# Performance work log

Measured on AMD Instinct MI355X. Metric: run time of the kernel, lower is better.

The kernel has to match this reference:

```python
import jax, jax.numpy as jnp
import numpy as np

SQ, B, NP, HN = 2048, 2, 16, 64  # [seq, batch, heads, head_dim]

def setup_inputs() -> dict:
    key = jax.random.key(0)
    kq, kk, kv = jax.random.split(key, 3)
    return {
        "query": jax.random.normal(kq, (SQ, B, NP, HN), dtype=jnp.float32),
        "key":   jax.random.normal(kk, (SQ, B, NP, HN), dtype=jnp.float32),
        "value": jax.random.normal(kv, (SQ, B, NP, HN), dtype=jnp.float32),
    }

def reference(query, key, value):
    sq, b, nheads, hn = query.shape
    # NOTE: original module computes norm_factor=sqrt(hn) but never applies it;
    # scores are UNscaled QK^T, replicated faithfully here.
    scores = jnp.einsum('sbnh,tbnh->bnst', query, key)          # [b, np, sq, sk]
    probs = jax.nn.softmax(scores, axis=-1)                      # mask=None -> plain softmax
    # dropout is deterministic (train=False default) -> identity
    context = jnp.einsum('bnst,tbnh->sbnh', probs, value)        # [sq, b, np, hn]
    return context.reshape(sq, b, nheads * hn).astype(jnp.float32)
```

## Files before the change

### kernel.cpp

```cpp
#include <hip/hip_runtime.h>
#include <math.h>
#include <stdint.h>

#define SQ 2048
#define NBH 32
#define HN 64
#define BQ 128
#define BK 64
#define NT (SQ/BK)
#define TOK 2048
#define HSTRIDE (SQ*HN)

typedef _Float16 half2v __attribute__((ext_vector_type(2)));
typedef _Float16 half4v __attribute__((ext_vector_type(4)));
typedef _Float16 half8v __attribute__((ext_vector_type(8)));
typedef float f32x16 __attribute__((ext_vector_type(16)));

__device__ __forceinline__ void async16(const void* g, void* l) {
  __builtin_amdgcn_global_load_lds(
      (const __attribute__((address_space(1))) void*)g,
      (__attribute__((address_space(3))) void*)l, 16, 0, 0);
}

__global__ __launch_bounds__(256) void prep_k(const float* __restrict__ K,
                                              _Float16* __restrict__ Kh) {
  const int t = threadIdx.x;
  const int head = blockIdx.y;
  const int key = blockIdx.x * 64 + (t >> 2);
  const int c0 = (t & 3) * 2;
  const float* src = K + (size_t)key * TOK + head * HN + c0 * 8;
  float4 a = *(const float4*)src;
  float4 b = *(const float4*)(src + 4);
  float4 c = *(const float4*)(src + 8);
  float4 d = *(const float4*)(src + 12);
  half8v h0, h1;
  h0[0]=(_Float16)a.x; h0[1]=(_Float16)a.y; h0[2]=(_Float16)a.z; h0[3]=(_Float16)a.w;
  h0[4]=(_Float16)b.x; h0[5]=(_Float16)b.y; h0[6]=(_Float16)b.z; h0[7]=(_Float16)b.w;
  h1[0]=(_Float16)c.x; h1[1]=(_Float16)c.y; h1[2]=(_Float16)c.z; h1[3]=(_Float16)c.w;
  h1[4]=(_Float16)d.x; h1[5]=(_Float16)d.y; h1[6]=(_Float16)d.z; h1[7]=(_Float16)d.w;
  _Float16* row = Kh + (size_t)head * HSTRIDE + (size_t)key * 64;
  *(half8v*)&row[((c0    ) ^ (key & 7)) * 8] = h0;
  *(half8v*)&row[((c0 + 1) ^ (key & 7)) * 8] = h1;
}

__global__ __launch_bounds__(256) void prep_v(const float* __restrict__ V,
                                              _Float16* __restrict__ Vt) {
  __shared__ _Float16 vs[HN * 64];
  const int t = threadIdx.x;
  const int head = blockIdx.y;
  const int kt = blockIdx.x * 64;
  const int kl = (t >> 3) * 2;
  const int db = (t & 7) * 8;
  const float* src = V + (size_t)(kt + kl) * TOK + head * HN + db;
  float4 a0 = *(const float4*)src;
  float4 a1 = *(const float4*)(src + 4);
  float4 b0 = *(const float4*)(src + TOK);
  float4 b1 = *(const float4*)(src + TOK + 4);
  const float av[8] = {a0.x,a0.y,a0.z,a0.w,a1.x,a1.y,a1.z,a1.w};
  const float bv[8] = {b0.x,b0.y,b0.z,b0.w,b1.x,b1.y,b1.z,b1.w};
  const int u = kl >> 2;
  #pragma unroll
  for (int j = 0; j < 8; ++j) {
    const int dim = db + j;
    const int pos = u ^ (dim & 15);
    half2v h; h[0] = (_Float16)av[j]; h[1] = (_Float16)bv[j];
    *(half2v*)&vs[dim * 64 + pos * 4 + (kl & 3)] = h;
  }
  __syncthreads();
  const int dim = t >> 2;
  const int q = (t & 3) ^ (dim & 3);
  const _Float16* srow = &vs[dim * 64 + q * 16];
  _Float16* drow = Vt + (size_t)head * HSTRIDE + (size_t)dim * SQ + kt + q * 16;
  *(half8v*)&drow[0] = *(const half8v*)&srow[0];
  *(half8v*)&drow[8] = *(const half8v*)&srow[8];
}

__global__ __launch_bounds__(256, 2)
void fattn_mfma(const float* __restrict__ Q, const _Float16* __restrict__ Kh,
                const _Float16* __restrict__ Vt, float* __restrict__ O) {
  __shared__ __align__(16) _Float16 kbf[2][BK * 64];
  __shared__ __align__(16) _Float16 vtf[2][HN * 64];

  const int t = threadIdx.x;
  const int lane = t & 63;
  const int w = t >> 6;
  const int h2 = lane >> 5;
  const int l31 = lane & 31;
  const int q0 = blockIdx.x * BQ + w * 32;
  const int head = blockIdx.y;
  const _Float16* Kp = Kh + (size_t)head * HSTRIDE;
  const _Float16* Vp = Vt + (size_t)head * HSTRIDE;

  half8v qf[4];
  {
    const float* qp = Q + (size_t)(q0 + l31) * TOK + head * HN + 8 * h2;
    #pragma unroll
    for (int ks = 0; ks < 4; ++ks) {
      float4 a = *(const float4*)(qp + 16 * ks);
      float4 b = *(const float4*)(qp + 16 * ks + 4);
      half8v f;
      f[0] = (_Float16)a.x; f[1] = (_Float16)a.y; f[2] = (_Float16)a.z; f[3] = (_Float16)a.w;
      f[4] = (_Float16)b.x; f[5] = (_Float16)b.y; f[6] = (_Float16)b.z; f[7] = (_Float16)b.w;
      qf[ks] = f;
    }
  }

  f32x16 acc0, acc1;
  #pragma unroll
  for (int r = 0; r < 16; ++r) { acc0[r] = 0.f; acc1[r] = 0.f; }
  float m_i = -INFINITY, l_i = 0.f;

  auto stage = [&](int it) {
    const int kt = it * BK;
    const int buf = it & 1;
    #pragma unroll
    for (int i = 0; i < 2; ++i) {
      const int off = w * 1024 + i * 512;
      async16(Kp + (size_t)kt * 64 + off + lane * 8, &kbf[buf][off]);
    }
    #pragma unroll
    for (int i = 0; i < 2; ++i) {
      const int off = w * 1024 + i * 512;
      const int eo = off + lane * 8;
      const int dim = eo >> 6, inner = eo & 63;
      async16(Vp + (size_t)dim * SQ + kt + inner, &vtf[buf][off]);
    }
  };

  stage(0);
  for (int it = 0; it < NT; ++it) {
    __syncthreads();
    if (it + 1 < NT) stage(it + 1);
    const int cur = it & 1;

    f32x16 sf0, sf1;
    {
      f32x16 c0, c1;
      #pragma unroll
      for (int r = 0; r < 16; ++r) { c0[r] = 0.f; c1[r] = 0.f; }
      #pragma unroll
      for (int ks = 0; ks < 4; ++ks) {
        const int pos = ((h2 + 2 * ks) ^ (l31 & 7)) * 8;
        half8v a0v = *(const half8v*)&kbf[cur][l31 * 64 + pos];
        half8v a1v = *(const half8v*)&kbf[cur][(l31 + 32) * 64 + pos];
        c0 = __builtin_amdgcn_mfma_f32_32x32x16_f16(a0v, qf[ks], c0, 0, 0, 0);
        c1 = __builtin_amdgcn_mfma_f32_32x32x16_f16(a1v, qf[ks], c1, 0, 0, 0);
      }
      sf0 = c0; sf1 = c1;
    }

    float mx = -INFINITY;
    #pragma unroll
    for (int r = 0; r < 16; ++r) mx = fmaxf(mx, fmaxf(sf0[r], sf1[r]));
    mx = fmaxf(mx, __shfl_xor(mx, 32, 64));
    const float mnew = fmaxf(m_i, mx);
    const float alpha = __expf(m_i - mnew);
    float rsum = 0.f;
    #pragma unroll
    for (int r = 0; r < 16; ++r) {
      float p0 = __expf(sf0[r] - mnew);
      float p1 = __expf(sf1[r] - mnew);
      sf0[r] = p0; sf1[r] = p1;
      rsum += p0 + p1;
    }
    rsum += __shfl_xor(rsum, 32, 64);
    l_i = l_i * alpha + rsum;
    m_i = mnew;
    #pragma unroll
    for (int r = 0; r < 16; ++r) { acc0[r] *= alpha; acc1[r] *= alpha; }

    #pragma unroll
    for (int ks = 0; ks < 4; ++ks) {
      const int rb = 8 * (ks & 1);
      const f32x16& s = (ks < 2) ? sf0 : sf1;
      union { half8v v8; half2v v2[4]; } pu;
      #pragma unroll
      for (int tt = 0; tt < 4; ++tt) {
        auto pk = __builtin_amdgcn_cvt_pkrtz(s[rb + 2 * tt], s[rb + 2 * tt + 1]);
        pu.v2[tt] = *(half2v*)&pk;
      }
      #pragma unroll
      for (int mbd = 0; mbd < 2; ++mbd) {
        const int dim = l31 + 32 * mbd;
        const int sw = dim & 15;
        union { half8v v8; half4v v4[2]; } au;
        au.v4[0] = *(const half4v*)&vtf[cur][dim * 64 + ((4 * ks + h2)     ^ sw) * 4];
        au.v4[1] = *(const half4v*)&vtf[cur][dim * 64 + ((4 * ks + 2 + h2) ^ sw) * 4];
        if (mbd == 0)
          acc0 = __builtin_amdgcn_mfma_f32_32x32x16_f16(au.v8, pu.v8, acc0, 0, 0, 0);
        else
          acc1 = __builtin_amdgcn_mfma_f32_32x32x16_f16(au.v8, pu.v8, acc1, 0, 0, 0);
      }
    }
  }

  const float invl = 1.f / l_i;
  float* orow = O + (size_t)(q0 + l31) * TOK + head * HN;
  #pragma unroll
  for (int r = 0; r < 16; ++r) {
    const int d = (r & 3) + 8 * (r >> 2) + 4 * h2;
    orow[d]      = acc0[r] * invl;
    orow[d + 32] = acc1[r] * invl;
  }
}

extern "C" void kernel_launch(void* const* d_in, const int* in_sizes, int n_in,
                              void* d_out, int out_size, void* d_ws, size_t ws_size,
                              hipStream_t stream) {
  const float* Q = (const float*)d_in[0];
  const float* K = (const float*)d_in[1];
  const float* V = (const float*)d_in[2];
  float* O = (float*)d_out;
  _Float16* Kh = (_Float16*)d_ws;
  _Float16* Vh = Kh + (size_t)NBH * HSTRIDE;
  prep_k<<<dim3(SQ / 64, NBH), 256, 0, stream>>>(K, Kh);
  prep_v<<<dim3(SQ / 64, NBH), 256, 0, stream>>>(V, Vh);
  fattn_mfma<<<dim3(SQ / BQ, NBH), 256, 0, stream>>>(Q, Kh, Vh, O);
}
```

Measured before the change: 159.7 us.

## Process 128 keys per iteration, use exp2 with prescaled Q, fuse K/V prep kernels

The attention loop now handles two 64-key tiles per iteration, which halves the number of barriers and online-softmax rescale steps and doubles the LDS staging buffers. Q is prescaled by log2(e) so the exponentials can use the native exp2 instruction. The separate K and V conversion kernels are merged into one launch to cut launch overhead. The cost is higher register and LDS use, which may lower occupancy, plus a small extra fp16 rounding from the prescaled Q.

```diff
diff --git a/kernel.cpp b/kernel.cpp
--- a/kernel.cpp
+++ b/kernel.cpp
@@ -7,7 +7,8 @@
 #define HN 64
 #define BQ 128
 #define BK 64
-#define NT (SQ/BK)
+#define BK2 128
+#define NP2 (SQ/BK2)
 #define TOK 2048
 #define HSTRIDE (SQ*HN)
 
@@ -22,64 +23,72 @@
       (__attribute__((address_space(3))) void*)l, 16, 0, 0);
 }
 
-__global__ __launch_bounds__(256) void prep_k(const float* __restrict__ K,
-                                              _Float16* __restrict__ Kh) {
-  const int t = threadIdx.x;
-  const int head = blockIdx.y;
-  const int key = blockIdx.x * 64 + (t >> 2);
-  const int c0 = (t & 3) * 2;
-  const float* src = K + (size_t)key * TOK + head * HN + c0 * 8;
-  float4 a = *(const float4*)src;
-  float4 b = *(const float4*)(src + 4);
-  float4 c = *(const float4*)(src + 8);
-  float4 d = *(const float4*)(src + 12);
-  half8v h0, h1;
-  h0[0]=(_Float16)a.x; h0[1]=(_Float16)a.y; h0[2]=(_Float16)a.z; h0[3]=(_Float16)a.w;
-  h0[4]=(_Float16)b.x; h0[5]=(_Float16)b.y; h0[6]=(_Float16)b.z; h0[7]=(_Float16)b.w;
-  h1[0]=(_Float16)c.x; h1[1]=(_Float16)c.y; h1[2]=(_Float16)c.z; h1[3]=(_Float16)c.w;
-  h1[4]=(_Float16)d.x; h1[5]=(_Float16)d.y; h1[6]=(_Float16)d.z; h1[7]=(_Float16)d.w;
-  _Float16* row = Kh + (size_t)head * HSTRIDE + (size_t)key * 64;
-  *(half8v*)&row[((c0    ) ^ (key & 7)) * 8] = h0;
-  *(half8v*)&row[((c0 + 1) ^ (key & 7)) * 8] = h1;
-}
-
-__global__ __launch_bounds__(256) void prep_v(const float* __restrict__ V,
-                                              _Float16* __restrict__ Vt) {
+__device__ __forceinline__ float fexp2(float x) {
+#if __has_builtin(__builtin_amdgcn_exp2f)
+  return __builtin_amdgcn_exp2f(x);
+#else
+  return exp2f(x);
+#endif
+}
+
+__global__ __launch_bounds__(256) void prep_kv(const float* __restrict__ K,
+                                               const float* __restrict__ V,
+                                               _Float16* __restrict__ Kh,
+                                               _Float16* __restrict__ Vt) {
   __shared__ _Float16 vs[HN * 64];
   const int t = threadIdx.x;
   const int head = blockIdx.y;
-  const int kt = blockIdx.x * 64;
-  const int kl = (t >> 3) * 2;
-  const int db = (t & 7) * 8;
-  const float* src = V + (size_t)(kt + kl) * TOK + head * HN + db;
-  float4 a0 = *(const float4*)src;
-  float4 a1 = *(const float4*)(src + 4);
-  float4 b0 = *(const float4*)(src + TOK);
-  float4 b1 = *(const float4*)(src + TOK + 4);
-  const float av[8] = {a0.x,a0.y,a0.z,a0.w,a1.x,a1.y,a1.z,a1.w};
-  const float bv[8] = {b0.x,b0.y,b0.z,b0.w,b1.x,b1.y,b1.z,b1.w};
-  const int u = kl >> 2;
-  #pragma unroll
-  for (int j = 0; j < 8; ++j) {
-    const int dim = db + j;
-    const int pos = u ^ (dim & 15);
-    half2v h; h[0] = (_Float16)av[j]; h[1] = (_Float16)bv[j];
-    *(half2v*)&vs[dim * 64 + pos * 4 + (kl & 3)] = h;
-  }
-  __syncthreads();
-  const int dim = t >> 2;
-  const int q = (t & 3) ^ (dim & 3);
-  const _Float16* srow = &vs[dim * 64 + q * 16];
-  _Float16* drow = Vt + (size_t)head * HSTRIDE + (size_t)dim * SQ + kt + q * 16;
-  *(half8v*)&drow[0] = *(const half8v*)&srow[0];
-  *(half8v*)&drow[8] = *(const half8v*)&srow[8];
+  {
+    const int key = blockIdx.x * 64 + (t >> 2);
+    const int c0 = (t & 3) * 2;
+    const float* src = K + (size_t)key * TOK + head * HN + c0 * 8;
+    float4 a = *(const float4*)src;
+    float4 b = *(const float4*)(src + 4);
+    float4 c = *(const float4*)(src + 8);
+    float4 d = *(const float4*)(src + 12);
+    half8v h0, h1;
+    h0[0]=(_Float16)a.x; h0[1]=(_Float16)a.y; h0[2]=(_Float16)a.z; h0[3]=(_Float16)a.w;
+    h0[4]=(_Float16)b.x; h0[5]=(_Float16)b.y; h0[6]=(_Float16)b.z; h0[7]=(_Float16)b.w;
+    h1[0]=(_Float16)c.x; h1[1]=(_Float16)c.y; h1[2]=(_Float16)c.z; h1[3]=(_Float16)c.w;
+    h1[4]=(_Float16)d.x; h1[5]=(_Float16)d.y; h1[6]=(_Float16)d.z; h1[7]=(_Float16)d.w;
+    _Float16* row = Kh + (size_t)head * HSTRIDE + (size_t)key * 64;
+    *(half8v*)&row[((c0    ) ^ (key & 7)) * 8] = h0;
+    *(half8v*)&row[((c0 + 1) ^ (key & 7)) * 8] = h1;
+  }
+  {
+    const int kt = blockIdx.x * 64;
+    const int kl = (t >> 3) * 2;
+    const int db = (t & 7) * 8;
+    const float* src = V + (size_t)(kt + kl) * TOK + head * HN + db;
+    float4 a0 = *(const float4*)src;
+    float4 a1 = *(const float4*)(src + 4);
+    float4 b0 = *(const float4*)(src + TOK);
+    float4 b1 = *(const float4*)(src + TOK + 4);
+    const float av[8] = {a0.x,a0.y,a0.z,a0.w,a1.x,a1.y,a1.z,a1.w};
+    const float bv[8] = {b0.x,b0.y,b0.z,b0.w,b1.x,b1.y,b1.z,b1.w};
+    const int u = kl >> 2;
+    #pragma unroll
+    for (int j = 0; j < 8; ++j) {
+      const int dim = db + j;
+      const int pos = u ^ (dim & 15);
+      half2v h; h[0] = (_Float16)av[j]; h[1] = (_Float16)bv[j];
+      *(half2v*)&vs[dim * 64 + pos * 4 + (kl & 3)] = h;
+    }
+    __syncthreads();
+    const int dim = t >> 2;
+    const int q = (t & 3) ^ (dim & 3);
+    const _Float16* srow = &vs[dim * 64 + q * 16];
+    _Float16* drow = Vt + (size_t)head * HSTRIDE + (size_t)dim * SQ + kt + q * 16;
+    *(half8v*)&drow[0] = *(const half8v*)&srow[0];
+    *(half8v*)&drow[8] = *(const half8v*)&srow[8];
+  }
 }
 
 __global__ __launch_bounds__(256, 2)
 void fattn_mfma(const float* __restrict__ Q, const _Float16* __restrict__ Kh,
                 const _Float16* __restrict__ Vt, float* __restrict__ O) {
-  __shared__ __align__(16) _Float16 kbf[2][BK * 64];
-  __shared__ __align__(16) _Float16 vtf[2][HN * 64];
+  __shared__ __align__(16) _Float16 kbf[2][2 * BK * 64];
+  __shared__ __align__(16) _Float16 vtf[2][2 * HN * 64];
 
   const int t = threadIdx.x;
   const int lane = t & 63;
@@ -94,13 +103,14 @@
   half8v qf[4];
   {
     const float* qp = Q + (size_t)(q0 + l31) * TOK + head * HN + 8 * h2;
+    const float s = 1.44269504088896f;
     #pragma unroll
     for (int ks = 0; ks < 4; ++ks) {
       float4 a = *(const float4*)(qp + 16 * ks);
       float4 b = *(const float4*)(qp + 16 * ks + 4);
       half8v f;
-      f[0] = (_Float16)a.x; f[1] = (_Float16)a.y; f[2] = (_Float16)a.z; f[3] = (_Float16)a.w;
-      f[4] = (_Float16)b.x; f[5] = (_Float16)b.y; f[6] = (_Float16)b.z; f[7] = (_Float16)b.w;
+      f[0] = (_Float16)(s*a.x); f[1] = (_Float16)(s*a.y); f[2] = (_Float16)(s*a.z); f[3] = (_Float16)(s*a.w);
+      f[4] = (_Float16)(s*b.x); f[5] = (_Float16)(s*b.y); f[6] = (_Float16)(s*b.z); f[7] = (_Float16)(s*b.w);
       qf[ks] = f;
     }
   }
@@ -110,58 +120,68 @@
   for (int r = 0; r < 16; ++r) { acc0[r] = 0.f; acc1[r] = 0.f; }
   float m_i = -INFINITY, l_i = 0.f;
 
-  auto stage = [&](int it) {
-    const int kt = it * BK;
-    const int buf = it & 1;
-    #pragma unroll
-    for (int i = 0; i < 2; ++i) {
-      const int off = w * 1024 + i * 512;
-      async16(Kp + (size_t)kt * 64 + off + lane * 8, &kbf[buf][off]);
-    }
-    #pragma unroll
-    for (int i = 0; i < 2; ++i) {
-      const int off = w * 1024 + i * 512;
-      const int eo = off + lane * 8;
-      const int dim = eo >> 6, inner = eo & 63;
-      async16(Vp + (size_t)dim * SQ + kt + inner, &vtf[buf][off]);
-    }
+  auto stage = [&](int p) {
+    const int buf = p & 1;
+    const size_t kt = (size_t)p * BK2;
+    #pragma unroll
+    for (int i = 0; i < 4; ++i) {
+      const int off = w * 512 + i * 2048;
+      async16(Kp + kt * 64 + off + lane * 8, &kbf[buf][off]);
+    }
+    #pragma unroll
+    for (int tl = 0; tl < 2; ++tl)
+      #pragma unroll
+      for (int i = 0; i < 2; ++i) {
+        const int off = w * 1024 + i * 512;
+        const int eo = off + lane * 8;
+        const int dim = eo >> 6, inner = eo & 63;
+        async16(Vp + (size_t)dim * SQ + kt + tl * 64 + inner,
+                &vtf[buf][tl * 4096 + off]);
+      }
   };
 
   stage(0);
-  for (int it = 0; it < NT; ++it) {
+  for (int p = 0; p < NP2; ++p) {
     __syncthreads();
-    if (it + 1 < NT) stage(it + 1);
-    const int cur = it & 1;
-
-    f32x16 sf0, sf1;
+    if (p + 1 < NP2) stage(p + 1);
+    const int cur = p & 1;
+
+    f32x16 sa0, sa1, sb0, sb1;
     {
-      f32x16 c0, c1;
-      #pragma unroll
-      for (int r = 0; r < 16; ++r) { c0[r] = 0.f; c1[r] = 0.f; }
+      f32x16 c0, c1, d0, d1;
+      #pragma unroll
+      for (int r = 0; r < 16; ++r) { c0[r]=0.f; c1[r]=0.f; d0[r]=0.f; d1[r]=0.f; }
       #pragma unroll
       for (int ks = 0; ks < 4; ++ks) {
         const int pos = ((h2 + 2 * ks) ^ (l31 & 7)) * 8;
         half8v a0v = *(const half8v*)&kbf[cur][l31 * 64 + pos];
         half8v a1v = *(const half8v*)&kbf[cur][(l31 + 32) * 64 + pos];
+        half8v b0v = *(const half8v*)&kbf[cur][4096 + l31 * 64 + pos];
+        half8v b1v = *(const half8v*)&kbf[cur][4096 + (l31 + 32) * 64 + pos];
         c0 = __builtin_amdgcn_mfma_f32_32x32x16_f16(a0v, qf[ks], c0, 0, 0, 0);
         c1 = __builtin_amdgcn_mfma_f32_32x32x16_f16(a1v, qf[ks], c1, 0, 0, 0);
+        d0 = __builtin_amdgcn_mfma_f32_32x32x16_f16(b0v, qf[ks], d0, 0, 0, 0);
+        d1 = __builtin_amdgcn_mfma_f32_32x32x16_f16(b1v, qf[ks], d1, 0, 0, 0);
       }
-      sf0 = c0; sf1 = c1;
+      sa0 = c0; sa1 = c1; sb0 = d0; sb1 = d1;
     }
 
     float mx = -INFINITY;
     #pragma unroll
-    for (int r = 0; r < 16; ++r) mx = fmaxf(mx, fmaxf(sf0[r], sf1[r]));
+    for (int r = 0; r < 16; ++r)
+      mx = fmaxf(mx, fmaxf(fmaxf(sa0[r], sa1[r]), fmaxf(sb0[r], sb1[r])));
     mx = fmaxf(mx, __shfl_xor(mx, 32, 64));
     const float mnew = fmaxf(m_i, mx);
-    const float alpha = __expf(m_i - mnew);
+    const float alpha = fexp2(m_i - mnew);
     float rsum = 0.f;
     #pragma unroll
     for (int r = 0; r < 16; ++r) {
-      float p0 = __expf(sf0[r] - mnew);
-      float p1 = __expf(sf1[r] - mnew);
-      sf0[r] = p0; sf1[r] = p1;
-      rsum += p0 + p1;
+      float p0 = fexp2(sa0[r] - mnew);
+      float p1 = fexp2(sa1[r] - mnew);
+      float p2 = fexp2(sb0[r] - mnew);
+      float p3 = fexp2(sb1[r] - mnew);
+      sa0[r] = p0; sa1[r] = p1; sb0[r] = p2; sb1[r] = p3;
+      rsum += (p0 + p1) + (p2 + p3);
     }
     rsum += __shfl_xor(rsum, 32, 64);
     l_i = l_i * alpha + rsum;
@@ -170,26 +190,30 @@
     for (int r = 0; r < 16; ++r) { acc0[r] *= alpha; acc1[r] *= alpha; }
 
     #pragma unroll
-    for (int ks = 0; ks < 4; ++ks) {
-      const int rb = 8 * (ks & 1);
-      const f32x16& s = (ks < 2) ? sf0 : sf1;
-      union { half8v v8; half2v v2[4]; } pu;
-      #pragma unroll
-      for (int tt = 0; tt < 4; ++tt) {
-        auto pk = __builtin_amdgcn_cvt_pkrtz(s[rb + 2 * tt], s[rb + 2 * tt + 1]);
-        pu.v2[tt] = *(half2v*)&pk;
-      }
-      #pragma unroll
-      for (int mbd = 0; mbd < 2; ++mbd) {
-        const int dim = l31 + 32 * mbd;
-        const int sw = dim & 15;
-        union { half8v v8; half4v v4[2]; } au;
-        au.v4[0] = *(const half4v*)&vtf[cur][dim * 64 + ((4 * ks + h2)     ^ sw) * 4];
-        au.v4[1] = *(const half4v*)&vtf[cur][dim * 64 + ((4 * ks + 2 + h2) ^ sw) * 4];
-        if (mbd == 0)
-          acc0 = __builtin_amdgcn_mfma_f32_32x32x16_f16(au.v8, pu.v8, acc0, 0, 0, 0);
-        else
-          acc1 = __builtin_amdgcn_mfma_f32_32x32x16_f16(au.v8, pu.v8, acc1, 0, 0, 0);
+    for (int tl = 0; tl < 2; ++tl) {
+      const int vbase = tl * 4096;
+      #pragma unroll
+      for (int ks = 0; ks < 4; ++ks) {
+        const int rb = 8 * (ks & 1);
+        const f32x16& s = tl ? ((ks < 2) ? sb0 : sb1) : ((ks < 2) ? sa0 : sa1);
+        union { half8v v8; half2v v2[4]; } pu;
+        #pragma unroll
+        for (int tt = 0; tt < 4; ++tt) {
+          auto pk = __builtin_amdgcn_cvt_pkrtz(s[rb + 2 * tt], s[rb + 2 * tt + 1]);
+          pu.v2[tt] = *(half2v*)&pk;
+        }
+        #pragma unroll
+        for (int mbd = 0; mbd < 2; ++mbd) {
+          const int dim = l31 + 32 * mbd;
+          const int sw = dim & 15;
+          union { half8v v8; half4v v4[2]; } au;
+          au.v4[0] = *(const half4v*)&vtf[cur][vbase + dim * 64 + ((4 * ks + h2)     ^ sw) * 4];
+          au.v4[1] = *(const half4v*)&vtf[cur][vbase + dim * 64 + ((4 * ks + 2 + h2) ^ sw) * 4];
+          if (mbd == 0)
+            acc0 = __builtin_amdgcn_mfma_f32_32x32x16_f16(au.v8, pu.v8, acc0, 0, 0, 0);
+          else
+            acc1 = __builtin_amdgcn_mfma_f32_32x32x16_f16(au.v8, pu.v8, acc1, 0, 0, 0);
+        }
       }
     }
   }
@@ -213,7 +237,6 @@
   float* O = (float*)d_out;
   _Float16* Kh = (_Float16*)d_ws;
   _Float16* Vh = Kh + (size_t)NBH * HSTRIDE;
-  prep_k<<<dim3(SQ / 64, NBH), 256, 0, stream>>>(K, Kh);
-  prep_v<<<dim3(SQ / 64, NBH), 256, 0, stream>>>(V, Vh);
+  prep_kv<<<dim3(SQ / 64, NBH), 256, 0, stream>>>(K, V, Kh, Vh);
   fattn_mfma<<<dim3(SQ / BQ, NBH), 256, 0, stream>>>(Q, Kh, Vh, O);
 }
```

Result: faster. 142.8 us (-10.6%).
